# Kernel tuning notes

Measured on AMD Instinct MI355X. Metric: run time of the kernel, lower is better.

## Reference

```python
import jax, jax.numpy as jnp
import numpy as np

T, B = 100, 256
NUM_IN, NUM_HID, NUM_OUT = 784, 512, 10
BETA = 0.95
THRESH = 1.0   # snntorch Leaky default threshold
SLOPE = 25.0   # surrogate.fast_sigmoid default slope

# Heaviside spike with fast_sigmoid surrogate gradient (snntorch semantics)
@jax.custom_vjp
def spike_fn(x):
    return (x > 0).astype(x.dtype)

def _spike_fwd(x):
    return spike_fn(x), x

def _spike_bwd(x, g):
    return (g / (SLOPE * jnp.abs(x) + 1.0) ** 2,)

spike_fn.defvjp(_spike_fwd, _spike_bwd)

def setup_inputs() -> dict:
    key = jax.random.key(0)
    ks = jax.random.split(key, 5)
    x = jax.random.normal(ks[0], (T, B, NUM_IN), dtype=jnp.float32)
    w1 = jax.random.normal(ks[1], (NUM_HID, NUM_IN), dtype=jnp.float32) / np.float32(np.sqrt(NUM_IN))
    b1 = jax.random.normal(ks[2], (NUM_HID,), dtype=jnp.float32) * 0.01
    w2 = jax.random.normal(ks[3], (NUM_OUT, NUM_HID), dtype=jnp.float32) / np.float32(np.sqrt(NUM_HID))
    b2 = jax.random.normal(ks[4], (NUM_OUT,), dtype=jnp.float32) * 0.01
    return {"x": x, "w1": w1, "b1": b1, "w2": w2, "b2": b2}

def _snn_forward(x, w1, b1, w2, b2):
    mem1_0 = jnp.zeros((B, NUM_HID), x.dtype)
    mem2_0 = jnp.zeros((B, NUM_OUT), x.dtype)

    def step(carry, xt):
        mem1, mem2 = carry
        # layer 1: Linear + Leaky (reset-by-subtraction, reset detached as in snntorch)
        cur1 = xt @ w1.T + b1
        reset1 = jax.lax.stop_gradient(spike_fn(mem1 - THRESH))
        mem1 = BETA * mem1 + cur1 - reset1 * THRESH
        spk1 = spike_fn(mem1 - THRESH)
        # layer 2
        cur2 = spk1 @ w2.T + b2
        reset2 = jax.lax.stop_gradient(spike_fn(mem2 - THRESH))
        mem2 = BETA * mem2 + cur2 - reset2 * THRESH
        spk2 = spike_fn(mem2 - THRESH)
        return (mem1, mem2), (cur2, spk2, spk1, mem2, mem1)

    _, ys = jax.lax.scan(step, (mem1_0, mem2_0), x)
    # ys = (cur_list, spk_list, spk_hidden_list, mem_list, mem_hidden_list), stacked over T
    return ys

def reference(x, w1, b1, w2, b2):
    return _snn_forward(x, w1, b1, w2, b2)
```

## Files before the change

### kernel.cpp

```cpp
#include <hip/hip_runtime.h>
#include <stdint.h>

#define T_STEPS 100
#define BATCH   256
#define NIN     784
#define NHID    512
#define NOUT    10


#define BM 128
#define BN 128
#define BK 8
#define PANEL_K 384

__global__ __launch_bounds__(256) void gemm1_dual(
    const float* __restrict__ X, const float* __restrict__ W,
    float* __restrict__ C1, float* __restrict__ C2)
{
    __shared__ float As[2][BK][BM + 4];
    __shared__ float Bs[2][BK][BN + 4];

    const int tid = threadIdx.x;
    const int bm  = blockIdx.x * BM;
    const int bn  = blockIdx.y * BN;
    const int kb  = blockIdx.z ? PANEL_K : 0;
    float* __restrict__ C = blockIdx.z ? C2 : C1;

    const int row  = tid >> 1;
    const int koff = (tid & 1) * 4;

    const int w    = tid >> 6;
    const int lane = tid & 63;
    const int tm   = (w & 1) * 64 + (lane & 7) * 8;
    const int tn   = (w >> 1) * 64 + (lane >> 3) * 8;

    float acc[8][8];
    #pragma unroll
    for (int i = 0; i < 8; ++i)
        #pragma unroll
        for (int j = 0; j < 8; ++j) acc[i][j] = 0.f;

    const float* Xp = X + (size_t)(bm + row) * NIN + kb + koff;
    const float* Wp = W + (size_t)(bn + row) * NIN + kb + koff;

    float4 pa = *(const float4*)(Xp);
    float4 pb = *(const float4*)(Wp);
    As[0][koff+0][row] = pa.x; As[0][koff+1][row] = pa.y;
    As[0][koff+2][row] = pa.z; As[0][koff+3][row] = pa.w;
    Bs[0][koff+0][row] = pb.x; Bs[0][koff+1][row] = pb.y;
    Bs[0][koff+2][row] = pb.z; Bs[0][koff+3][row] = pb.w;

    const int NITER = PANEL_K / BK;
    for (int it = 0; it < NITER; ++it) {
        const int cur = it & 1;
        __syncthreads();

        if (it + 1 < NITER) {
            const int k0 = (it + 1) * BK;
            pa = *(const float4*)(Xp + k0);
            pb = *(const float4*)(Wp + k0);
        }

        #pragma unroll
        for (int kk = 0; kk < BK; ++kk) {
            float4 av0 = *(const float4*)&As[cur][kk][tm];
            float4 av1 = *(const float4*)&As[cur][kk][tm + 4];
            float4 bv0 = *(const float4*)&Bs[cur][kk][tn];
            float4 bv1 = *(const float4*)&Bs[cur][kk][tn + 4];
            float a[8] = {av0.x, av0.y, av0.z, av0.w, av1.x, av1.y, av1.z, av1.w};
            float b[8] = {bv0.x, bv0.y, bv0.z, bv0.w, bv1.x, bv1.y, bv1.z, bv1.w};
            #pragma unroll
            for (int i = 0; i < 8; ++i)
                #pragma unroll
                for (int j = 0; j < 8; ++j)
                    acc[i][j] = fmaf(a[i], b[j], acc[i][j]);
        }

        if (it + 1 < NITER) {
            const int nxt = cur ^ 1;
            As[nxt][koff+0][row] = pa.x; As[nxt][koff+1][row] = pa.y;
            As[nxt][koff+2][row] = pa.z; As[nxt][koff+3][row] = pa.w;
            Bs[nxt][koff+0][row] = pb.x; Bs[nxt][koff+1][row] = pb.y;
            Bs[nxt][koff+2][row] = pb.z; Bs[nxt][koff+3][row] = pb.w;
        }
    }

    #pragma unroll
    for (int i = 0; i < 8; ++i) {
        size_t r = (size_t)(bm + tm + i) * NHID + bn + tn;
        *(float4*)&C[r]     = make_float4(acc[i][0], acc[i][1], acc[i][2], acc[i][3]);
        *(float4*)&C[r + 4] = make_float4(acc[i][4], acc[i][5], acc[i][6], acc[i][7]);
    }
}

__global__ __launch_bounds__(1024) void leaky_hidden_fused(
    float* __restrict__ mem_io,
    const float* c2,
    float* spk_out,
    const float* __restrict__ X,
    const float* __restrict__ W1,
    const float* __restrict__ b1)
{
    __shared__ float4 xs4[T_STEPS][4];
    __shared__ float  p1s[2][8][NHID];
    __shared__ float  p2s[2][8][NHID];

    const int tid = threadIdx.x;
    const int bb  = blockIdx.x;
    const size_t STRIDE = (size_t)BATCH * NHID;
    const size_t base   = (size_t)bb * NHID;

    if (tid < T_STEPS * 4) {
        const int t = tid >> 2, q = tid & 3;
        xs4[t][q] = *(const float4*)(X + (size_t)t * BATCH * NIN
                                       + (size_t)bb * NIN + 768 + q * 4);
    }

    const bool producer = (tid >= 512);
    const int  lane     = tid & 511;
    const size_t col    = base + lane;

    float wt[16];
    float bias = 0.f;
    float mem  = 0.f;

    if (producer) {
        const int p = tid - 512;
        const int s = p >> 8;
        const int q = p & 255;
        const float* src = s ? c2 : mem_io;
        float4 v[4];
        #pragma unroll
        for (int jj = 0; jj < 4; ++jj) {
            const int flat = q + 256 * jj;
            const int j = flat >> 7, f4 = flat & 127;
            v[jj] = *(const float4*)(src + base + 4 * f4 + (size_t)j * STRIDE);
        }
        #pragma unroll
        for (int jj = 0; jj < 4; ++jj) {
            const int flat = q + 256 * jj;
            const int j = flat >> 7, f4 = flat & 127;
            float* dst = s ? &p2s[0][j][4 * f4] : &p1s[0][j][4 * f4];
            *(float4*)dst = v[jj];
        }
    } else {
        const int h = lane;
        const float* wp = W1 + (size_t)h * NIN + 768;
        float4 w0  = *(const float4*)(wp);
        float4 w1v = *(const float4*)(wp + 4);
        float4 w2v = *(const float4*)(wp + 8);
        float4 w3v = *(const float4*)(wp + 12);
        wt[0]=w0.x;  wt[1]=w0.y;  wt[2]=w0.z;  wt[3]=w0.w;
        wt[4]=w1v.x; wt[5]=w1v.y; wt[6]=w1v.z; wt[7]=w1v.w;
        wt[8]=w2v.x; wt[9]=w2v.y; wt[10]=w2v.z; wt[11]=w2v.w;
        wt[12]=w3v.x; wt[13]=w3v.y; wt[14]=w3v.z; wt[15]=w3v.w;
        bias = b1[h];
    }

    __syncthreads();

    for (int c = 0; c <= 12; ++c) {
        if (producer) {
            if (c < 12) {
                const int t0n = (c + 1) * 8;
                const int nb  = (c + 1 == 12) ? 4 : 8;
                const int nIt = nb >> 1;
                const int p = tid - 512;
                const int s = p >> 8;
                const int q = p & 255;
                const float* src = s ? c2 : mem_io;
                const int pb = (c + 1) & 1;
                float4 v[4];
                #pragma unroll
                for (int jj = 0; jj < 4; ++jj) {
                    if (jj < nIt) {
                        const int flat = q + 256 * jj;
                        const int j = flat >> 7, f4 = flat & 127;
                        v[jj] = *(const float4*)(src + base + 4 * f4
                                                 + (size_t)(t0n + j) * STRIDE);
                    }
                }
                #pragma unroll
                for (int jj = 0; jj < 4; ++jj) {
                    if (jj < nIt) {
                        const int flat = q + 256 * jj;
                        const int j = flat >> 7, f4 = flat & 127;
                        float* dst = s ? &p2s[pb][j][4 * f4]
                                       : &p1s[pb][j][4 * f4];
                        *(float4*)dst = v[jj];
                    }
                }
            }
        } else {
            const int nt = (c == 12) ? 4 : 8;
            const int cb = c & 1;
            #pragma unroll
            for (int j = 0; j < 8; ++j) {
                if (j < nt) {
                    const int t = c * 8 + j;
                    const float p1 = p1s[cb][j][lane];
                    const float p2 = p2s[cb][j][lane];
                    float4 v0 = xs4[t][0], v1 = xs4[t][1];
                    float4 v2 = xs4[t][2], v3 = xs4[t][3];
                    float a = 0.f;
                    a = fmaf(v0.x, wt[0], a);  a = fmaf(v0.y, wt[1], a);
                    a = fmaf(v0.z, wt[2], a);  a = fmaf(v0.w, wt[3], a);
                    a = fmaf(v1.x, wt[4], a);  a = fmaf(v1.y, wt[5], a);
                    a = fmaf(v1.z, wt[6], a);  a = fmaf(v1.w, wt[7], a);
                    a = fmaf(v2.x, wt[8], a);  a = fmaf(v2.y, wt[9], a);
                    a = fmaf(v2.z, wt[10], a); a = fmaf(v2.w, wt[11], a);
                    a = fmaf(v3.x, wt[12], a); a = fmaf(v3.y, wt[13], a);
                    a = fmaf(v3.z, wt[14], a); a = fmaf(v3.w, wt[15], a);

                    const float cur = __fadd_rn(__fadd_rn(__fadd_rn(p1, p2), a), bias);
                    const float rst = (mem > 1.0f) ? 1.0f : 0.0f;
                    mem = __fsub_rn(__fadd_rn(__fmul_rn(0.95f, mem), cur), rst);

                    const size_t off = col + (size_t)t * STRIDE;
                    spk_out[off] = (mem > 1.0f) ? 1.0f : 0.0f;
                    mem_io[off]  = mem;
                }
            }
        }
        __syncthreads();
    }
}

__global__ __launch_bounds__(512) void gemm2_lout_fused(
    const float* __restrict__ spk1, const float* __restrict__ W2,
    const float* __restrict__ b2, float* __restrict__ cur2,
    float* __restrict__ spk2, float* __restrict__ mem2)
{
    __shared__ double ps [8][64][11];
    __shared__ double ps2[8][4][11];
    __shared__ float  c2s[T_STEPS][NOUT];

    const int tid  = threadIdx.x;
    const int w    = tid >> 6;
    const int lane = tid & 63;
    const int b    = blockIdx.x;

    float w2r[10][8];
    #pragma unroll
    for (int o = 0; o < NOUT; ++o) {
        float4 a0 = *(const float4*)(W2 + (size_t)o * NHID + 8 * lane);
        float4 a1 = *(const float4*)(W2 + (size_t)o * NHID + 8 * lane + 4);
        w2r[o][0]=a0.x; w2r[o][1]=a0.y; w2r[o][2]=a0.z; w2r[o][3]=a0.w;
        w2r[o][4]=a1.x; w2r[o][5]=a1.y; w2r[o][6]=a1.z; w2r[o][7]=a1.w;
    }

    for (int t = w; t < T_STEPS; t += 8) {
        const float* sp = spk1 + (size_t)t * (BATCH * NHID)
                               + (size_t)b * NHID + 8 * lane;
        float4 s0 = *(const float4*)(sp);
        float4 s1 = *(const float4*)(sp + 4);
        const float s[8] = {s0.x, s0.y, s0.z, s0.w, s1.x, s1.y, s1.z, s1.w};

        #pragma unroll
        for (int o = 0; o < NOUT; ++o) {
            double d = 0.0;
            #pragma unroll
            for (int j = 0; j < 8; ++j)
                d = fma((double)s[j], (double)w2r[o][j], d);
            ps[w][lane][o] = d;
        }
        asm volatile("s_waitcnt lgkmcnt(0)" ::: "memory");

        if (lane < 40) {
            const int o = lane >> 2, g = lane & 3;
            double d = 0.0;
            #pragma unroll
            for (int l2 = 0; l2 < 16; ++l2)
                d += ps[w][g * 16 + l2][o];
            ps2[w][g][o] = d;
        }
        asm volatile("s_waitcnt lgkmcnt(0)" ::: "memory");

        if (lane < 10) {
            const int o = lane;
            double d = ((ps2[w][0][o] + ps2[w][1][o]) + ps2[w][2][o])
                       + ps2[w][3][o];
            const float c = (float)(d + (double)b2[o]);
            cur2[(size_t)t * (BATCH * NOUT) + (size_t)b * NOUT + o] = c;
            c2s[t][o] = c;
        }
    }

    __syncthreads();

    if (tid < NOUT) {
        const int o = tid;
        float mem = 0.f;
        for (int t = 0; t < T_STEPS; ++t) {
            const float cur = c2s[t][o];
            const float rst = (mem > 1.0f) ? 1.0f : 0.0f;
            mem = __fsub_rn(__fadd_rn(__fmul_rn(0.95f, mem), cur), rst);
            const size_t off = (size_t)t * (BATCH * NOUT) + (size_t)b * NOUT + o;
            spk2[off] = (mem > 1.0f) ? 1.0f : 0.0f;
            mem2[off] = mem;
        }
    }
}

extern "C" void kernel_launch(void* const* d_in, const int* in_sizes, int n_in,
                              void* d_out, int out_size, void* d_ws, size_t ws_size,
                              hipStream_t stream) {
    const float* x  = (const float*)d_in[0];
    const float* w1 = (const float*)d_in[1];
    const float* b1 = (const float*)d_in[2];
    const float* w2 = (const float*)d_in[3];
    const float* b2 = (const float*)d_in[4];

    float* out = (float*)d_out;
    float* cur2_out = out;
    float* spk2_out = out + 256000;
    float* spk1_out = out + 512000;
    float* mem2_out = out + 13619200;
    float* mem1_out = out + 13875200;

    const int M = T_STEPS * BATCH;

    const size_t p2_bytes = (size_t)M * NHID * sizeof(float);
    float* p2buf = (d_ws != nullptr && ws_size >= p2_bytes)
                       ? (float*)d_ws : spk1_out;

    dim3 gp(M / BM, NHID / BN, 2);
    gemm1_dual<<<gp, 256, 0, stream>>>(x, w1, mem1_out, p2buf);

    leaky_hidden_fused<<<BATCH, 1024, 0, stream>>>(
        mem1_out, p2buf, spk1_out, x, w1, b1);

    gemm2_lout_fused<<<BATCH, 512, 0, stream>>>(
        spk1_out, w2, b2, cur2_out, spk2_out, mem2_out);
}
```

Before: 447.2 us.

## Fuse layer-2 GEMM and output leaky neuron into hidden leaky kernel via spike bitmasks

Removes the separate gemm2_lout kernel and folds it into the hidden-layer leaky kernel. Consumer warps publish each step's spikes as ballot bitmasks in shared memory. Producer warps, one chunk later, rebuild the spikes from those masks and compute the 10-output projection against W2 held in shared memory. This avoids re-reading the 52 MB spk1 tensor from global memory and saves one kernel launch. In exchange it adds shared memory (W2 plus the double-precision partial-sum buffers) that may reduce occupancy, and one extra loop iteration of producer work.

Measured after the change: 449.8 us. Within noise of the previous version (+0.6%).

```diff
diff --git a/kernel.cpp b/kernel.cpp
--- a/kernel.cpp
+++ b/kernel.cpp
@@ -93,17 +93,28 @@
     }
 }
 
-__global__ __launch_bounds__(1024) void leaky_hidden_fused(
+__global__ __launch_bounds__(1024) void leaky_g2_fused(
     float* __restrict__ mem_io,
-    const float* c2,
+    const float* c2p,
     float* spk_out,
     const float* __restrict__ X,
     const float* __restrict__ W1,
-    const float* __restrict__ b1)
+    const float* __restrict__ b1,
+    const float* __restrict__ W2,
+    const float* __restrict__ b2,
+    float* __restrict__ cur2,
+    float* __restrict__ spk2,
+    float* __restrict__ mem2)
 {
     __shared__ float4 xs4[T_STEPS][4];
     __shared__ float  p1s[2][8][NHID];
     __shared__ float  p2s[2][8][NHID];
+    __shared__ unsigned long long spkb[2][8][8];
+    __shared__ float  w2sl[NOUT * NHID];
+    __shared__ double ps [8][64][11];
+    __shared__ double ps2[8][4][11];
+    __shared__ float  c2s[T_STEPS][NOUT];
+    __shared__ float  b2s[NOUT];
 
     const int tid = threadIdx.x;
     const int bb  = blockIdx.x;
@@ -115,6 +126,8 @@
         xs4[t][q] = *(const float4*)(X + (size_t)t * BATCH * NIN
                                        + (size_t)bb * NIN + 768 + q * 4);
     }
+    for (int i = tid; i < NOUT * NHID; i += 1024) w2sl[i] = W2[i];
+    if (tid < NOUT) b2s[tid] = b2[tid];
 
     const bool producer = (tid >= 512);
     const int  lane     = tid & 511;
@@ -128,7 +141,7 @@
         const int p = tid - 512;
         const int s = p >> 8;
         const int q = p & 255;
-        const float* src = s ? c2 : mem_io;
+        const float* src = s ? c2p : mem_io;
         float4 v[4];
         #pragma unroll
         for (int jj = 0; jj < 4; ++jj) {
@@ -159,17 +172,20 @@
 
     __syncthreads();
 
-    for (int c = 0; c <= 12; ++c) {
+    for (int c = 0; c <= 13; ++c) {
         if (producer) {
+            const int p  = tid - 512;
+            const int pw = p >> 6;
+            const int pl = p & 63;
+
             if (c < 12) {
                 const int t0n = (c + 1) * 8;
                 const int nb  = (c + 1 == 12) ? 4 : 8;
                 const int nIt = nb >> 1;
-                const int p = tid - 512;
                 const int s = p >> 8;
                 const int q = p & 255;
-                const float* src = s ? c2 : mem_io;
-                const int pb = (c + 1) & 1;
+                const float* src = s ? c2p : mem_io;
+                const int pbuf = (c + 1) & 1;
                 float4 v[4];
                 #pragma unroll
                 for (int jj = 0; jj < 4; ++jj) {
@@ -185,15 +201,68 @@
                     if (jj < nIt) {
                         const int flat = q + 256 * jj;
                         const int j = flat >> 7, f4 = flat & 127;
-                        float* dst = s ? &p2s[pb][j][4 * f4]
-                                       : &p1s[pb][j][4 * f4];
+                        float* dst = s ? &p2s[pbuf][j][4 * f4]
+                                       : &p1s[pbuf][j][4 * f4];
                         *(float4*)dst = v[jj];
                     }
                 }
             }
-        } else {
+
+            if (c >= 1) {
+                const int cp  = c - 1;
+                const int ntp = (cp == 12) ? 4 : 8;
+                if (pw < ntp) {
+                    const int t   = cp * 8 + pw;
+                    const int cb2 = cp & 1;
+                    const unsigned long long mA = spkb[cb2][pw][pl >> 4];
+                    const unsigned long long mB = spkb[cb2][pw][4 + (pl >> 4)];
+                    const int sh = (4 * pl) & 63;
+                    float sv[8];
+                    #pragma unroll
+                    for (int j = 0; j < 4; ++j) {
+                        sv[j]     = ((mA >> (sh + j)) & 1ull) ? 1.0f : 0.0f;
+                        sv[4 + j] = ((mB >> (sh + j)) & 1ull) ? 1.0f : 0.0f;
+                    }
+                    #pragma unroll
+                    for (int o = 0; o < NOUT; ++o) {
+                        float4 wA = *(const float4*)&w2sl[o * NHID + 4 * pl];
+                        float4 wB = *(const float4*)&w2sl[o * NHID + 256 + 4 * pl];
+                        double d = 0.0;
+                        d = fma((double)sv[0], (double)wA.x, d);
+                        d = fma((double)sv[1], (double)wA.y, d);
+                        d = fma((double)sv[2], (double)wA.z, d);
+                        d = fma((double)sv[3], (double)wA.w, d);
+                        d = fma((double)sv[4], (double)wB.x, d);
+                        d = fma((double)sv[5], (double)wB.y, d);
+                        d = fma((double)sv[6], (double)wB.z, d);
+                        d = fma((double)sv[7], (double)wB.w, d);
+                        ps[pw][pl][o] = d;
+                    }
+                    asm volatile("s_waitcnt lgkmcnt(0)" ::: "memory");
+                    if (pl < 40) {
+                        const int o = pl >> 2, g = pl & 3;
+                        double d = 0.0;
+                        #pragma unroll
+                        for (int l2 = 0; l2 < 16; ++l2)
+                            d += ps[pw][g * 16 + l2][o];
+                        ps2[pw][g][o] = d;
+                    }
+                    asm volatile("s_waitcnt lgkmcnt(0)" ::: "memory");
+                    if (pl < 10) {
+                        const int o = pl;
+                        double d = ((ps2[pw][0][o] + ps2[pw][1][o])
+                                    + ps2[pw][2][o]) + ps2[pw][3][o];
+                        const float cv = (float)(d + (double)b2s[o]);
+                        cur2[(size_t)t * (BATCH * NOUT)
+                             + (size_t)bb * NOUT + o] = cv;
+                        c2s[t][o] = cv;
+                    }
+                }
+            }
+        } else if (c <= 12) {
             const int nt = (c == 12) ? 4 : 8;
             const int cb = c & 1;
+            const int cw = tid >> 6;
             #pragma unroll
             for (int j = 0; j < 8; ++j) {
                 if (j < nt) {
@@ -216,88 +285,29 @@
                     const float rst = (mem > 1.0f) ? 1.0f : 0.0f;
                     mem = __fsub_rn(__fadd_rn(__fmul_rn(0.95f, mem), cur), rst);
 
+                    const bool sp = (mem > 1.0f);
                     const size_t off = col + (size_t)t * STRIDE;
-                    spk_out[off] = (mem > 1.0f) ? 1.0f : 0.0f;
+                    spk_out[off] = sp ? 1.0f : 0.0f;
                     mem_io[off]  = mem;
+
+                    const unsigned long long msk = __ballot(sp);
+                    if ((tid & 63) == 0) spkb[cb][j][cw] = msk;
                 }
             }
         }
         __syncthreads();
     }
-}
-
-__global__ __launch_bounds__(512) void gemm2_lout_fused(
-    const float* __restrict__ spk1, const float* __restrict__ W2,
-    const float* __restrict__ b2, float* __restrict__ cur2,
-    float* __restrict__ spk2, float* __restrict__ mem2)
-{
-    __shared__ double ps [8][64][11];
-    __shared__ double ps2[8][4][11];
-    __shared__ float  c2s[T_STEPS][NOUT];
-
-    const int tid  = threadIdx.x;
-    const int w    = tid >> 6;
-    const int lane = tid & 63;
-    const int b    = blockIdx.x;
-
-    float w2r[10][8];
-    #pragma unroll
-    for (int o = 0; o < NOUT; ++o) {
-        float4 a0 = *(const float4*)(W2 + (size_t)o * NHID + 8 * lane);
-        float4 a1 = *(const float4*)(W2 + (size_t)o * NHID + 8 * lane + 4);
-        w2r[o][0]=a0.x; w2r[o][1]=a0.y; w2r[o][2]=a0.z; w2r[o][3]=a0.w;
-        w2r[o][4]=a1.x; w2r[o][5]=a1.y; w2r[o][6]=a1.z; w2r[o][7]=a1.w;
-    }
-
-    for (int t = w; t < T_STEPS; t += 8) {
-        const float* sp = spk1 + (size_t)t * (BATCH * NHID)
-                               + (size_t)b * NHID + 8 * lane;
-        float4 s0 = *(const float4*)(sp);
-        float4 s1 = *(const float4*)(sp + 4);
-        const float s[8] = {s0.x, s0.y, s0.z, s0.w, s1.x, s1.y, s1.z, s1.w};
-
-        #pragma unroll
-        for (int o = 0; o < NOUT; ++o) {
-            double d = 0.0;
-            #pragma unroll
-            for (int j = 0; j < 8; ++j)
-                d = fma((double)s[j], (double)w2r[o][j], d);
-            ps[w][lane][o] = d;
-        }
-        asm volatile("s_waitcnt lgkmcnt(0)" ::: "memory");
-
-        if (lane < 40) {
-            const int o = lane >> 2, g = lane & 3;
-            double d = 0.0;
-            #pragma unroll
-            for (int l2 = 0; l2 < 16; ++l2)
-                d += ps[w][g * 16 + l2][o];
-            ps2[w][g][o] = d;
-        }
-        asm volatile("s_waitcnt lgkmcnt(0)" ::: "memory");
-
-        if (lane < 10) {
-            const int o = lane;
-            double d = ((ps2[w][0][o] + ps2[w][1][o]) + ps2[w][2][o])
-                       + ps2[w][3][o];
-            const float c = (float)(d + (double)b2[o]);
-            cur2[(size_t)t * (BATCH * NOUT) + (size_t)b * NOUT + o] = c;
-            c2s[t][o] = c;
-        }
-    }
-
-    __syncthreads();
 
     if (tid < NOUT) {
         const int o = tid;
-        float mem = 0.f;
+        float m2 = 0.f;
         for (int t = 0; t < T_STEPS; ++t) {
             const float cur = c2s[t][o];
-            const float rst = (mem > 1.0f) ? 1.0f : 0.0f;
-            mem = __fsub_rn(__fadd_rn(__fmul_rn(0.95f, mem), cur), rst);
-            const size_t off = (size_t)t * (BATCH * NOUT) + (size_t)b * NOUT + o;
-            spk2[off] = (mem > 1.0f) ? 1.0f : 0.0f;
-            mem2[off] = mem;
+            const float rst = (m2 > 1.0f) ? 1.0f : 0.0f;
+            m2 = __fsub_rn(__fadd_rn(__fmul_rn(0.95f, m2), cur), rst);
+            const size_t off = (size_t)t * (BATCH * NOUT) + (size_t)bb * NOUT + o;
+            spk2[off] = (m2 > 1.0f) ? 1.0f : 0.0f;
+            mem2[off] = m2;
         }
     }
 }
@@ -327,9 +337,7 @@
     dim3 gp(M / BM, NHID / BN, 2);
     gemm1_dual<<<gp, 256, 0, stream>>>(x, w1, mem1_out, p2buf);
 
-    leaky_hidden_fused<<<BATCH, 1024, 0, stream>>>(
-        mem1_out, p2buf, spk1_out, x, w1, b1);
-
-    gemm2_lout_fused<<<BATCH, 512, 0, stream>>>(
-        spk1_out, w2, b2, cur2_out, spk2_out, mem2_out);
+    leaky_g2_fused<<<BATCH, 1024, 0, stream>>>(
+        mem1_out, p2buf, spk1_out, x, w1, b1, w2, b2,
+        cur2_out, spk2_out, mem2_out);
 }
```
